# Kernel tuning notes

Hardware: AMD Instinct MI355X
Metric: run time of the kernel (lower is better)

Reference implementation:

```python
import jax, jax.numpy as jnp
import numpy as np

DIM = 128
HOP = 2
NEIGH = [12, 2]  # neighbor_num per hop
ALPHA = 0.2      # leaky-relu slope
NUM_NODE = 50000
B, S = 128, 50
STDV = 1.0 / np.sqrt(DIM)


def _leaky(x):
    return jnp.where(x >= 0, x, ALPHA * x)


def _local_agg(h, adj, a_local):
    # h: [B,S,D], adj: [B,S,S] ints in 0..4, a_local: [4,D]
    a_in = h[:, :, None, :] * h[:, None, :, :]            # [B,S,S,D]
    e = _leaky(jnp.einsum('bijd,kd->kbij', a_in, a_local))  # [4,B,S,S]
    att = jnp.full(adj.shape, -9e15, dtype=h.dtype)
    for k in range(4):
        att = jnp.where(adj == k + 1, e[k], att)
    att = jax.nn.softmax(att, axis=-1)
    return jnp.einsum('bij,bjd->bid', att, h)


def _global_agg(self_v, neigh_v, extra_v, w1, w2, w3, bias):
    # self_v: [B,N,D], neigh_v: [B,N,K,D], extra_v: [B,N,D]
    a = _leaky(jnp.einsum('bnkd,de->bnke', extra_v[:, :, None, :] * neigh_v, w1))
    a = jnp.einsum('bnke,e->bnk', a, w2)
    a = jax.nn.softmax(a, axis=-1)
    agg = jnp.einsum('bnk,bnkd->bnd', a, neigh_v)
    out = jnp.concatenate([self_v, agg], axis=-1) @ w3 + bias
    return jax.nn.relu(out)


def setup_inputs() -> dict:
    key = jax.random.key(0)
    ks = jax.random.split(key, 12)
    u = lambda k, shp: jax.random.uniform(k, shp, jnp.float32, -STDV, STDV)
    return {
        'inputs': jax.random.randint(ks[0], (B, S), 0, NUM_NODE),
        'adj': jax.random.randint(ks[1], (B, S, S), 0, 5),
        'mask_item': jnp.ones((B, S), dtype=jnp.int32),
        'item': jax.random.randint(ks[2], (B, S), 0, NUM_NODE),
        'first_adj': jax.random.randint(ks[3], (B, S * NEIGH[0]), 0, NUM_NODE),
        'adj_all': jax.random.randint(ks[4], (NUM_NODE, 2), 0, NUM_NODE),
        'embedding': u(ks[5], (NUM_NODE, DIM)),
        'a_local': u(ks[6], (4, DIM)),
        'gw1': u(ks[7], (HOP, DIM, DIM)),
        'gw2': u(ks[8], (HOP, DIM)),
        'gw3': u(ks[9], (HOP, 2 * DIM, DIM)),
        'gbias': u(ks[10], (HOP, DIM)),
    }


def reference(inputs, adj, mask_item, item, first_adj, adj_all,
              embedding, a_local, gw1, gw2, gw3, gbias):
    b, s = inputs.shape
    h = embedding[inputs]                                  # [B,S,D]
    h_local = _local_agg(h, adj, a_local)

    m = mask_item.astype(embedding.dtype)[..., None]       # [B,S,1]
    item_emb = embedding[item] * m
    sum_item = jnp.sum(item_emb, 1) / jnp.sum(m, 1)        # [B,D]
    sess = sum_item[:, None, :]                            # [B,1,D]

    # multi-hop neighbor sampling
    neigh1 = first_adj.reshape(b, s * NEIGH[0])            # [B, 600]
    neigh2 = adj_all[neigh1.reshape(-1)].reshape(b, s * NEIGH[0] * NEIGH[1])  # [B,1200]
    ev = [embedding[inputs], embedding[neigh1], embedding[neigh2]]

    for n_hop in range(HOP):
        nxt = []
        for hop in range(HOP - n_hop):
            neigh_v = ev[hop + 1].reshape(b, -1, NEIGH[hop], DIM)
            extra_v = jnp.broadcast_to(sess, (b, ev[hop].shape[1], DIM))
            nxt.append(_global_agg(ev[hop], neigh_v, extra_v,
                                   gw1[n_hop], gw2[n_hop], gw3[n_hop], gbias[n_hop]))
        ev = nxt
    h_global = ev[0].reshape(b, s, DIM)

    # dropout is identity at eval
    return h_local + h_global
```

## Files before the change

### kernel.cpp

```cpp
#include <hip/hip_runtime.h>
#include <stdint.h>

typedef unsigned short ushort_t;
typedef __attribute__((ext_vector_type(8))) short bf16x8;
typedef __attribute__((ext_vector_type(4))) float f32x4;

#define B_   128
#define S_   50
#define D_   128
#define ALPHA_ 0.2f

__device__ __forceinline__ float bf2f(ushort_t u){
  return __uint_as_float(((uint32_t)u) << 16);
}
__device__ __forceinline__ ushort_t f2bf(float f){
  uint32_t x = __float_as_uint(f);
  x = (x + 0x7fffu + ((x >> 16) & 1u)) >> 16;
  return (ushort_t)x;
}
__device__ __forceinline__ float leaky(float x){ return x >= 0.f ? x : ALPHA_*x; }

__device__ __forceinline__ int detect_flag_block(const uint32_t* __restrict__ emb_raw){
  __shared__ int flg;
  if (threadIdx.x == 0){
    int ok = 1;
    for (int i = 0; i < 64; i++){
      uint32_t lo = emb_raw[i] & 0xffffu;
      uint32_t ex = (lo >> 7) & 0xFFu;
      if (!(lo == 0u || (ex >= 64u && ex <= 126u))) ok = 0;
    }
    flg = ok;
  }
  __syncthreads();
  return flg;
}

__global__ void cvt_all(const void* __restrict__ p0, const void* __restrict__ p1,
                        const void* __restrict__ p2, const void* __restrict__ p3,
                        const void* __restrict__ p4, const void* __restrict__ p5,
                        ushort_t* __restrict__ dst){
  int flag = detect_flag_block((const uint32_t*)p0);
  const int seg_end[6] = {6400000, 6400512, 6433280, 6433536, 6499072, 6499328};
  int base = (blockIdx.x*256 + threadIdx.x) * 4;
  if (base >= 6499328) return;
  int s = 0;
  while (base >= seg_end[s]) s++;
  int segbase = (s == 0) ? 0 : seg_end[s-1];
  const void* src = (s==0)?p0:(s==1)?p1:(s==2)?p2:(s==3)?p3:(s==4)?p4:p5;
  int off = base - segbase;
  union { ushort_t u[4]; uint2 d2; } o;
  if (flag){
    o.d2 = *(const uint2*)((const ushort_t*)src + off);
  } else {
    float4 v = *(const float4*)((const float*)src + off);
    o.u[0] = f2bf(v.x); o.u[1] = f2bf(v.y); o.u[2] = f2bf(v.z); o.u[3] = f2bf(v.w);
  }
  *(uint2*)(dst + base) = o.d2;
}

__global__ void prep_frags(const void* __restrict__ emb_raw,
                           const void* __restrict__ w1r, const void* __restrict__ w3r,
                           uint4* __restrict__ w1f, uint4* __restrict__ w3f){
  int flag = detect_flag_block((const uint32_t*)emb_raw);
  int id = blockIdx.x*256 + threadIdx.x;
  if (id >= 12288) return;
  if (id < 4096){
    int h = id >> 11, i = id & 2047;
    int kt = i >> 9, rem = i & 511, t = rem >> 6, ln = rem & 63;
    int q = ln >> 4, c = ln & 15;
    union { ushort_t u[8]; uint4 q4; } e;
    #pragma unroll
    for (int j = 0; j < 8; j++){
      int idx = h*16384 + (32*kt + q*8 + j)*128 + 16*t + c;
      e.u[j] = flag ? ((const ushort_t*)w1r)[idx] : f2bf(((const float*)w1r)[idx]);
    }
    w1f[h*2048 + i] = e.q4;
  } else {
    int id2 = id - 4096;
    int h = id2 >> 12, i = id2 & 4095;
    int kt = i >> 9, rem = i & 511, t = rem >> 6, ln = rem & 63;
    int q = ln >> 4, c = ln & 15;
    union { ushort_t u[8]; uint4 q4; } e;
    #pragma unroll
    for (int j = 0; j < 8; j++){
      int idx = h*32768 + (32*kt + q*8 + j)*128 + 16*t + c;
      e.u[j] = flag ? ((const ushort_t*)w3r)[idx] : f2bf(((const float*)w3r)[idx]);
    }
    w3f[h*4096 + i] = e.q4;
  }
}

__global__ __launch_bounds__(256) void sess_local(
    const int* __restrict__ inputs, const int* __restrict__ adj,
    const int* __restrict__ item, const int* __restrict__ mask,
    const ushort_t* __restrict__ emb, const ushort_t* __restrict__ alocb,
    ushort_t* __restrict__ sessb, ushort_t* __restrict__ hlb){
  int blk = blockIdx.x;
  int tid = threadIdx.x;
  if (blk >= 512){
    int b = (blk - 512)*2 + (tid >> 7);
    int d = tid & 127;
    float acc = 0.f, den = 0.f;
    for (int s = 0; s < S_; s++){
      float fm = (float)mask[b*S_ + s];
      int id = item[b*S_ + s];
      acc += fm * bf2f(emb[(size_t)id*D_ + d]);
      den += fm;
    }
    sessb[b*D_ + d] = f2bf(acc / den);
    return;
  }
  __shared__ ushort_t hS[64][136];
  __shared__ float    attS[16][68];
  __shared__ int      sids[64];
  int b  = blk >> 2;
  int mi = blk & 3;
  if (tid < 64) sids[tid] = (tid < S_) ? inputs[b*S_ + tid] : 0;
  __syncthreads();
  for (int idx = tid; idx < 64*16; idx += 256){
    int j = idx >> 4, ch = idx & 15;
    uint4 v = {0u, 0u, 0u, 0u};
    if (j < S_) v = *(const uint4*)(emb + (size_t)sids[j]*D_ + ch*8);
    *(uint4*)(&hS[j][ch*8]) = v;
  }
  for (int idx = tid; idx < 16*64; idx += 256)
    attS[idx >> 6][idx & 63] = -9.0e15f;
  __syncthreads();

  int lane = tid & 63, wv = tid >> 6;
  int q = lane >> 4, c = lane & 15;

  f32x4 Eacc[4];
  #pragma unroll
  for (int ni = 0; ni < 4; ni++) Eacc[ni] = (f32x4){0.f,0.f,0.f,0.f};
  #pragma unroll
  for (int kt = 0; kt < 4; kt++){
    uint4 av = *(const uint4*)(alocb + wv*D_ + kt*32 + q*8);
    const uint32_t* ap = (const uint32_t*)&av;
    uint4 hv = *(const uint4*)(&hS[mi*16 + c][kt*32 + q*8]);
    const uint32_t* hp = (const uint32_t*)&hv;
    union { ushort_t u[8]; bf16x8 v; } afr;
    #pragma unroll
    for (int p = 0; p < 4; p++){
      float x0 = __uint_as_float(hp[p] << 16)         * __uint_as_float(ap[p] << 16);
      float x1 = __uint_as_float(hp[p] & 0xffff0000u) * __uint_as_float(ap[p] & 0xffff0000u);
      afr.u[2*p]   = f2bf(x0);
      afr.u[2*p+1] = f2bf(x1);
    }
    #pragma unroll
    for (int ni = 0; ni < 4; ni++){
      union { uint4 q4; bf16x8 v; } bfr;
      bfr.q4 = *(const uint4*)(&hS[ni*16 + c][kt*32 + q*8]);
      Eacc[ni] = __builtin_amdgcn_mfma_f32_16x16x32_bf16(afr.v, bfr.v, Eacc[ni], 0,0,0);
    }
  }
  const int* adjb = adj + (size_t)b*S_*S_;
  #pragma unroll
  for (int ni = 0; ni < 4; ni++){
    int j = ni*16 + c;
    #pragma unroll
    for (int r = 0; r < 4; r++){
      int i = mi*16 + q*4 + r;
      if (i < S_ && j < S_){
        int kk = adjb[i*S_ + j];
        if (kk == wv + 1) attS[q*4 + r][j] = leaky(Eacc[ni][r]);
      }
    }
  }
  __syncthreads();
  if (tid < 16){
    int i = mi*16 + tid;
    if (i < S_){
      float mx = -__builtin_inff();
      for (int j = 0; j < S_; j++) mx = fmaxf(mx, attS[tid][j]);
      float s = 0.f;
      for (int j = 0; j < S_; j++){ float e = __expf(attS[tid][j] - mx); attS[tid][j] = e; s += e; }
      float inv = 1.f / s;
      for (int j = 0; j < S_; j++) attS[tid][j] *= inv;
      for (int j = S_; j < 64; j++) attS[tid][j] = 0.f;
    } else {
      for (int j = 0; j < 64; j++) attS[tid][j] = 0.f;
    }
  }
  __syncthreads();
  f32x4 Pacc[2];
  Pacc[0] = (f32x4){0.f,0.f,0.f,0.f};
  Pacc[1] = (f32x4){0.f,0.f,0.f,0.f};
  #pragma unroll
  for (int kt = 0; kt < 2; kt++){
    union { ushort_t u[8]; bf16x8 v; } afr;
    const float* arow = &attS[c][kt*32 + q*8];
    #pragma unroll
    for (int j = 0; j < 8; j++) afr.u[j] = f2bf(arow[j]);
    #pragma unroll
    for (int nn = 0; nn < 2; nn++){
      int ni = 2*wv + nn;
      union { ushort_t u[8]; bf16x8 v; } bfr;
      #pragma unroll
      for (int jj = 0; jj < 8; jj++)
        bfr.u[jj] = hS[kt*32 + q*8 + jj][ni*16 + c];
      Pacc[nn] = __builtin_amdgcn_mfma_f32_16x16x32_bf16(afr.v, bfr.v, Pacc[nn], 0,0,0);
    }
  }
  #pragma unroll
  for (int nn = 0; nn < 2; nn++){
    int d = (2*wv + nn)*16 + c;
    #pragma unroll
    for (int r = 0; r < 4; r++){
      int i = mi*16 + q*4 + r;
      if (i < S_) hlb[((size_t)b*S_ + i)*D_ + d] = f2bf(Pacc[nn][r]);
    }
  }
}

__global__ __launch_bounds__(256) void score_mfma_ab(
    const ushort_t* __restrict__ sessb, const ushort_t* __restrict__ emb,
    const int* __restrict__ neigh1, const int* __restrict__ adj_all,
    const uint4* __restrict__ w1f, const ushort_t* __restrict__ w2,
    float* __restrict__ score, int nA){
  __shared__ uint4 bfrag[2048];
  int tid = threadIdx.x;
  for (int i = tid; i < 2048; i += 256) bfrag[i] = w1f[i];
  __syncthreads();
  int lane = tid & 63, wave = tid >> 6;
  int m = lane & 15, q = lane >> 4;
  float w2v[8];
  #pragma unroll
  for (int t = 0; t < 8; t++) w2v[t] = bf2f(w2[16*t + m]);

  for (int it = 0; it < 2; it++){
    int row_base = blockIdx.x*128 + it*64 + wave*16;
    int row = row_base + m;
    const ushort_t* nrow; int b;
    if (row < nA){
      nrow = emb + (size_t)neigh1[row]*D_;
      b = row / 600;
    } else {
      int r2 = row - nA;
      nrow = emb + (size_t)adj_all[(size_t)neigh1[r2>>1]*2 + (r2&1)]*D_;
      b = r2 / 1200;
    }
    const ushort_t* srow = sessb + (size_t)b*D_;

    f32x4 acc[8];
    #pragma unroll
    for (int t = 0; t < 8; t++) acc[t] = (f32x4){0.f,0.f,0.f,0.f};
    #pragma unroll
    for (int kt = 0; kt < 4; kt++){
      uint4 nv = *(const uint4*)(nrow + kt*32 + q*8);
      uint4 sv = *(const uint4*)(srow + kt*32 + q*8);
      const uint32_t* np = (const uint32_t*)&nv;
      const uint32_t* sp = (const uint32_t*)&sv;
      union { ushort_t u[8]; bf16x8 v; } afr;
      #pragma unroll
      for (int p = 0; p < 4; p++){
        uint32_t n2 = np[p], s2 = sp[p];
        float a0 = __uint_as_float(n2 << 16)          * __uint_as_float(s2 << 16);
        float a1 = __uint_as_float(n2 & 0xffff0000u)  * __uint_as_float(s2 & 0xffff0000u);
        afr.u[2*p]   = f2bf(a0);
        afr.u[2*p+1] = f2bf(a1);
      }
      #pragma unroll
      for (int t = 0; t < 8; t++){
        union { uint4 q4; bf16x8 v; } bfr;
        bfr.q4 = bfrag[(kt*8 + t)*64 + lane];
        acc[t] = __builtin_amdgcn_mfma_f32_16x16x32_bf16(afr.v, bfr.v, acc[t], 0, 0, 0);
      }
    }
    #pragma unroll
    for (int r = 0; r < 4; r++){
      float s = 0.f;
      #pragma unroll
      for (int t = 0; t < 8; t++) s += leaky(acc[t][r]) * w2v[t];
      s += __shfl_xor(s, 1, 64);
      s += __shfl_xor(s, 2, 64);
      s += __shfl_xor(s, 4, 64);
      s += __shfl_xor(s, 8, 64);
      if (m == 0) score[row_base + q*4 + r] = s;
    }
  }
}

__global__ __launch_bounds__(256) void score_mfma_c(
    const ushort_t* __restrict__ sessb, const ushort_t* __restrict__ out1,
    const uint4* __restrict__ w1f, const ushort_t* __restrict__ w2,
    float* __restrict__ score){
  __shared__ uint4 bfrag[2048];
  int tid = threadIdx.x;
  for (int i = tid; i < 2048; i += 256) bfrag[i] = w1f[i];
  __syncthreads();
  int lane = tid & 63, wave = tid >> 6;
  int m = lane & 15, q = lane >> 4;
  float w2v[8];
  #pragma unroll
  for (int t = 0; t < 8; t++) w2v[t] = bf2f(w2[16*t + m]);
  for (int it = 0; it < 2; it++){
    int row_base = blockIdx.x*128 + it*64 + wave*16;
    int row = row_base + m;
    const ushort_t* nrow = out1 + (size_t)row*D_;
    int b = row / 600;
    const ushort_t* srow = sessb + (size_t)b*D_;
    f32x4 acc[8];
    #pragma unroll
    for (int t = 0; t < 8; t++) acc[t] = (f32x4){0.f,0.f,0.f,0.f};
    #pragma unroll
    for (int kt = 0; kt < 4; kt++){
      uint4 nv = *(const uint4*)(nrow + kt*32 + q*8);
      uint4 sv = *(const uint4*)(srow + kt*32 + q*8);
      const uint32_t* np = (const uint32_t*)&nv;
      const uint32_t* sp = (const uint32_t*)&sv;
      union { ushort_t u[8]; bf16x8 v; } afr;
      #pragma unroll
      for (int p = 0; p < 4; p++){
        uint32_t n2 = np[p], s2 = sp[p];
        float a0 = __uint_as_float(n2 << 16)          * __uint_as_float(s2 << 16);
        float a1 = __uint_as_float(n2 & 0xffff0000u)  * __uint_as_float(s2 & 0xffff0000u);
        afr.u[2*p]   = f2bf(a0);
        afr.u[2*p+1] = f2bf(a1);
      }
      #pragma unroll
      for (int t = 0; t < 8; t++){
        union { uint4 q4; bf16x8 v; } bfr;
        bfr.q4 = bfrag[(kt*8 + t)*64 + lane];
        acc[t] = __builtin_amdgcn_mfma_f32_16x16x32_bf16(afr.v, bfr.v, acc[t], 0, 0, 0);
      }
    }
    #pragma unroll
    for (int r = 0; r < 4; r++){
      float s = 0.f;
      #pragma unroll
      for (int t = 0; t < 8; t++) s += leaky(acc[t][r]) * w2v[t];
      s += __shfl_xor(s, 1, 64);
      s += __shfl_xor(s, 2, 64);
      s += __shfl_xor(s, 4, 64);
      s += __shfl_xor(s, 8, 64);
      if (m == 0) score[row_base + q*4 + r] = s;
    }
  }
}

template<int K>
__device__ __forceinline__ void softmaxK(const float* __restrict__ sc, float att[K]){
  float mx = -__builtin_inff();
  #pragma unroll
  for (int k = 0; k < K; k++){ att[k] = sc[k]; mx = fmaxf(mx, att[k]); }
  float s = 0.f;
  #pragma unroll
  for (int k = 0; k < K; k++){ att[k] = __expf(att[k] - mx); s += att[k]; }
  float inv = 1.f / s;
  #pragma unroll
  for (int k = 0; k < K; k++) att[k] *= inv;
}

template<int K>
__device__ __forceinline__ void out_tile(
    int lane, const uint4* __restrict__ afrag,
    const ushort_t* __restrict__ sptr, const ushort_t* const nptr[K],
    const float att[K], f32x4 acc[8]){
  int q = lane >> 4;
  #pragma unroll
  for (int kt = 0; kt < 8; kt++){
    union { ushort_t u[8]; uint4 q4; bf16x8 v; } bfr;
    if (kt < 4){
      bfr.q4 = *(const uint4*)(sptr + kt*32 + q*8);
    } else {
      float g[8] = {0,0,0,0,0,0,0,0};
      #pragma unroll
      for (int k = 0; k < K; k++){
        uint4 nv = *(const uint4*)(nptr[k] + (kt-4)*32 + q*8);
        const uint32_t* np = (const uint32_t*)&nv;
        #pragma unroll
        for (int p = 0; p < 4; p++){
          g[2*p]   = fmaf(att[k], __uint_as_float(np[p] << 16),         g[2*p]);
          g[2*p+1] = fmaf(att[k], __uint_as_float(np[p] & 0xffff0000u), g[2*p+1]);
        }
      }
      #pragma unroll
      for (int j = 0; j < 8; j++) bfr.u[j] = f2bf(g[j]);
    }
    #pragma unroll
    for (int t = 0; t < 8; t++){
      union { uint4 q4; bf16x8 v; } af;
      af.q4 = afrag[(kt*8 + t)*64 + lane];
      acc[t] = __builtin_amdgcn_mfma_f32_16x16x32_bf16(af.v, bfr.v, acc[t], 0, 0, 0);
    }
  }
}

__global__ __launch_bounds__(512) void out_mfma_ab(
    const float* __restrict__ score, const int* __restrict__ idx,
    const int* __restrict__ nbr, const int* __restrict__ adj_all,
    const ushort_t* __restrict__ emb, const uint4* __restrict__ w3f,
    const ushort_t* __restrict__ bias,
    ushort_t* __restrict__ o0c, ushort_t* __restrict__ out1c,
    int nA, int nTot, int scoreBbase){
  __shared__ uint4 afrag[4096];
  int tid = threadIdx.x;
  for (int i = tid; i < 4096; i += 512) afrag[i] = w3f[i];
  __syncthreads();
  int lane = tid & 63, wave = tid >> 6;
  int mrow = lane & 15, q = lane >> 4;
  float bv[8][4];
  #pragma unroll
  for (int t = 0; t < 8; t++){
    const ushort_t* bp = bias + 16*t + q*4;
    #pragma unroll
    for (int r = 0; r < 4; r++) bv[t][r] = bf2f(bp[r]);
  }
  int row_base = blockIdx.x*128 + wave*16;
  int row = row_base + mrow;
  bool active = row < nTot;
  int rowc = active ? row : (nTot - 1);
  bool isA = rowc < nA;
  f32x4 acc[8];
  #pragma unroll
  for (int t = 0; t < 8; t++) acc[t] = (f32x4){0.f,0.f,0.f,0.f};
  if (isA){
    const ushort_t* sptr = emb + (size_t)idx[rowc]*D_;
    const ushort_t* nptr[12];
    #pragma unroll
    for (int k = 0; k < 12; k++) nptr[k] = emb + (size_t)nbr[rowc*12 + k]*D_;
    float att[12];
    softmaxK<12>(score + (size_t)rowc*12, att);
    out_tile<12>(lane, afrag, sptr, nptr, att, acc);
  } else {
    int rB = rowc - nA;
    const ushort_t* sptr = emb + (size_t)nbr[rB]*D_;
    const ushort_t* nptr[2];
    #pragma unroll
    for (int k = 0; k < 2; k++) nptr[k] = emb + (size_t)adj_all[(size_t)nbr[rB]*2 + k]*D_;
    float att[2];
    softmaxK<2>(score + scoreBbase + (size_t)rB*2, att);
    out_tile<2>(lane, afrag, sptr, nptr, att, acc);
  }
  if (active){
    ushort_t* dst = isA ? (o0c + (size_t)row*D_) : (out1c + (size_t)(row - nA)*D_);
    #pragma unroll
    for (int t = 0; t < 8; t++){
      int col0 = 16*t + q*4;
      union { ushort_t u[4]; uint2 d2; } pk;
      #pragma unroll
      for (int r = 0; r < 4; r++) pk.u[r] = f2bf(fmaxf(acc[t][r] + bv[t][r], 0.f));
      *(uint2*)(dst + col0) = pk.d2;
    }
  }
}

__global__ __launch_bounds__(512) void out_mfma_c(
    const float* __restrict__ score, const ushort_t* __restrict__ out1,
    const ushort_t* __restrict__ selfsrc, const uint4* __restrict__ w3f,
    const ushort_t* __restrict__ bias,
    const ushort_t* __restrict__ addsrc, float* __restrict__ outf, int nrows){
  __shared__ uint4 afrag[4096];
  int tid = threadIdx.x;
  for (int i = tid; i < 4096; i += 512) afrag[i] = w3f[i];
  __syncthreads();
  int lane = tid & 63, wave = tid >> 6;
  int mrow = lane & 15, q = lane >> 4;
  float bv[8][4];
  #pragma unroll
  for (int t = 0; t < 8; t++){
    const ushort_t* bp = bias + 16*t + q*4;
    #pragma unroll
    for (int r = 0; r < 4; r++) bv[t][r] = bf2f(bp[r]);
  }
  int row_base = blockIdx.x*128 + wave*16;
  int row = row_base + mrow;
  bool active = row < nrows;
  int rowc = active ? row : (nrows - 1);
  const ushort_t* sptr = selfsrc + (size_t)rowc*D_;
  const ushort_t* nptr[12];
  #pragma unroll
  for (int k = 0; k < 12; k++) nptr[k] = out1 + (size_t)(rowc*12 + k)*D_;
  float att[12];
  softmaxK<12>(score + (size_t)rowc*12, att);
  f32x4 acc[8];
  #pragma unroll
  for (int t = 0; t < 8; t++) acc[t] = (f32x4){0.f,0.f,0.f,0.f};
  out_tile<12>(lane, afrag, sptr, nptr, att, acc);
  if (active){
    #pragma unroll
    for (int t = 0; t < 8; t++){
      int col0 = 16*t + q*4;
      float v[4];
      const ushort_t* ap = addsrc + (size_t)row*D_ + col0;
      #pragma unroll
      for (int r = 0; r < 4; r++)
        v[r] = fmaxf(acc[t][r] + bv[t][r], 0.f) + bf2f(ap[r]);
      *(f32x4*)(outf + (size_t)row*D_ + col0) = (f32x4){v[0], v[1], v[2], v[3]};
    }
  }
}

extern "C" void kernel_launch(void* const* d_in, const int* in_sizes, int n_in,
                              void* d_out, int out_size, void* d_ws, size_t ws_size,
                              hipStream_t stream) {
  const int* inputs    = (const int*)d_in[0];
  const int* adj       = (const int*)d_in[1];
  const int* mask_item = (const int*)d_in[2];
  const int* item      = (const int*)d_in[3];
  const int* first_adj = (const int*)d_in[4];
  const int* adj_all   = (const int*)d_in[5];

  char* ws = (char*)d_ws;
  size_t o = 0;
  ushort_t* emb_b  = (ushort_t*)(ws + o); o += 12800000;
  ushort_t* alocb  = (ushort_t*)(ws + o); o += 1024;
  ushort_t* gw1b   = (ushort_t*)(ws + o); o += 65536;
  ushort_t* gw2b   = (ushort_t*)(ws + o); o += 512;
  ushort_t* gw3b   = (ushort_t*)(ws + o); o += 131072;
  ushort_t* gbb    = (ushort_t*)(ws + o); o += 512;
  ushort_t* sessb  = (ushort_t*)(ws + o); o += 32768;
  ushort_t* hlb    = (ushort_t*)(ws + o); o += 1638400;
  uint4*    w1f    = (uint4*)(ws + o);    o += 65536;
  uint4*    w3f    = (uint4*)(ws + o);    o += 131072;
  size_t fixed = o;
  (void)gw1b; (void)gw3b;
  int CHB = 16;
  if      (ws_size >= fixed + (size_t)128*173600) CHB = 128;
  else if (ws_size >= fixed + (size_t)64 *173600) CHB = 64;
  else if (ws_size >= fixed + (size_t)32 *173600) CHB = 32;
  ushort_t* out1c = (ushort_t*)(ws + o);  o += (size_t)CHB*153600;
  ushort_t* o0c   = (ushort_t*)(ws + o);  o += (size_t)CHB*12800;
  float*    score = (float*)(ws + o);

  float* outp = (float*)d_out;

  cvt_all<<<(6499328/4 + 255)/256, 256, 0, stream>>>(d_in[6], d_in[7], d_in[8], d_in[9],
                                                     d_in[10], d_in[11], emb_b);
  prep_frags<<<48, 256, 0, stream>>>(d_in[6], d_in[8], d_in[10], w1f, w3f);

  sess_local<<<576, 256, 0, stream>>>(inputs, adj, item, mask_item,
                                      emb_b, alocb, sessb, hlb);

  int nchunk = B_ / CHB;
  for (int c = 0; c < nchunk; c++){
    int b0 = c * CHB;
    const int* fadj  = first_adj + (size_t)b0 * 600;
    const ushort_t* sbc = sessb + (size_t)b0 * D_;
    ushort_t*  hlc   = hlb  + (size_t)b0 * 50 * D_;
    float*     outc  = outp + (size_t)b0 * 50 * D_;
    int nA600 = CHB*600, nA50 = CHB*50, nTot = CHB*650;

    score_mfma_ab<<<(3*nA600)/128, 256, 0, stream>>>(sbc, emb_b, fadj, adj_all,
                                                     w1f, gw2b, score, nA600);
    out_mfma_ab<<<(nTot + 127)/128, 512, 0, stream>>>(score, inputs + b0*50, fadj, adj_all,
                                                      emb_b, w3f, gbb, o0c, out1c,
                                                      nA50, nTot, nA600);
    score_mfma_c<<<nA600/128, 256, 0, stream>>>(sbc, out1c, w1f + 2048, gw2b + 128, score);
    out_mfma_c<<<(nA50 + 127)/128, 512, 0, stream>>>(score, out1c, o0c,
                                                     w3f + 4096, gbb + 128,
                                                     hlc, outc, nA50);
  }
}
```

Baseline: 199.4 us.

## Precompute per-node W3 projections and fuse setup kernels into one launch

Merges the conversion, fragment-prep, session-mean and local-attention kernels into a single launch. The local and session blocks now read the raw embedding directly instead of waiting for the converted copy. It also adds a path that projects every embedding row through both halves of W3 up front (Tt, Tb), so hop-0 output becomes a softmax-weighted gather of projected rows instead of a per-row MFMA. That path projects all 50k nodes rather than only the gathered ones, and needs extra workspace; when workspace is short it falls back to the old chunked path.

```diff
diff --git a/kernel.cpp b/kernel.cpp
--- a/kernel.cpp
+++ b/kernel.cpp
@@ -35,180 +35,259 @@
   return flg;
 }
 
-__global__ void cvt_all(const void* __restrict__ p0, const void* __restrict__ p1,
-                        const void* __restrict__ p2, const void* __restrict__ p3,
-                        const void* __restrict__ p4, const void* __restrict__ p5,
-                        ushort_t* __restrict__ dst){
-  int flag = detect_flag_block((const uint32_t*)p0);
-  const int seg_end[6] = {6400000, 6400512, 6433280, 6433536, 6499072, 6499328};
-  int base = (blockIdx.x*256 + threadIdx.x) * 4;
-  if (base >= 6499328) return;
-  int s = 0;
-  while (base >= seg_end[s]) s++;
-  int segbase = (s == 0) ? 0 : seg_end[s-1];
-  const void* src = (s==0)?p0:(s==1)?p1:(s==2)?p2:(s==3)?p3:(s==4)?p4:p5;
-  int off = base - segbase;
-  union { ushort_t u[4]; uint2 d2; } o;
-  if (flag){
-    o.d2 = *(const uint2*)((const ushort_t*)src + off);
-  } else {
-    float4 v = *(const float4*)((const float*)src + off);
-    o.u[0] = f2bf(v.x); o.u[1] = f2bf(v.y); o.u[2] = f2bf(v.z); o.u[3] = f2bf(v.w);
-  }
-  *(uint2*)(dst + base) = o.d2;
-}
-
-__global__ void prep_frags(const void* __restrict__ emb_raw,
-                           const void* __restrict__ w1r, const void* __restrict__ w3r,
-                           uint4* __restrict__ w1f, uint4* __restrict__ w3f){
-  int flag = detect_flag_block((const uint32_t*)emb_raw);
-  int id = blockIdx.x*256 + threadIdx.x;
-  if (id >= 12288) return;
-  if (id < 4096){
-    int h = id >> 11, i = id & 2047;
-    int kt = i >> 9, rem = i & 511, t = rem >> 6, ln = rem & 63;
-    int q = ln >> 4, c = ln & 15;
-    union { ushort_t u[8]; uint4 q4; } e;
-    #pragma unroll
-    for (int j = 0; j < 8; j++){
-      int idx = h*16384 + (32*kt + q*8 + j)*128 + 16*t + c;
-      e.u[j] = flag ? ((const ushort_t*)w1r)[idx] : f2bf(((const float*)w1r)[idx]);
-    }
-    w1f[h*2048 + i] = e.q4;
-  } else {
-    int id2 = id - 4096;
-    int h = id2 >> 12, i = id2 & 4095;
-    int kt = i >> 9, rem = i & 511, t = rem >> 6, ln = rem & 63;
-    int q = ln >> 4, c = ln & 15;
-    union { ushort_t u[8]; uint4 q4; } e;
-    #pragma unroll
-    for (int j = 0; j < 8; j++){
-      int idx = h*32768 + (32*kt + q*8 + j)*128 + 16*t + c;
-      e.u[j] = flag ? ((const ushort_t*)w3r)[idx] : f2bf(((const float*)w3r)[idx]);
-    }
-    w3f[h*4096 + i] = e.q4;
-  }
-}
-
-__global__ __launch_bounds__(256) void sess_local(
+#define NLOCAL_ 512
+#define NSESS_  64
+#define NCVT_   6347
+#define NPREP_  48
+
+__global__ __launch_bounds__(256) void k1(
     const int* __restrict__ inputs, const int* __restrict__ adj,
     const int* __restrict__ item, const int* __restrict__ mask,
-    const ushort_t* __restrict__ emb, const ushort_t* __restrict__ alocb,
-    ushort_t* __restrict__ sessb, ushort_t* __restrict__ hlb){
-  int blk = blockIdx.x;
-  int tid = threadIdx.x;
-  if (blk >= 512){
-    int b = (blk - 512)*2 + (tid >> 7);
+    const void* __restrict__ p0, const void* __restrict__ p1,
+    const void* __restrict__ p2, const void* __restrict__ p3,
+    const void* __restrict__ p4, const void* __restrict__ p5,
+    ushort_t* __restrict__ emb_b, uint4* __restrict__ w1f, uint4* __restrict__ w3f,
+    ushort_t* __restrict__ sessb, ushort_t* __restrict__ hlb)
+{
+  int blk = blockIdx.x, tid = threadIdx.x;
+  int flag = detect_flag_block((const uint32_t*)p0);
+
+  if (blk < NLOCAL_){
+    __shared__ ushort_t hS[64][136];
+    __shared__ float    attS[16][68];
+    __shared__ int      sids[64];
+    __shared__ ushort_t alS[512];
+    int b  = blk >> 2;
+    int mi = blk & 3;
+    if (tid < 64) sids[tid] = (tid < S_) ? inputs[b*S_ + tid] : 0;
+    for (int i = tid; i < 512; i += 256)
+      alS[i] = flag ? ((const ushort_t*)p1)[i] : f2bf(((const float*)p1)[i]);
+    __syncthreads();
+    if (flag){
+      const ushort_t* e16 = (const ushort_t*)p0;
+      for (int idx = tid; idx < 64*16; idx += 256){
+        int j = idx >> 4, ch = idx & 15;
+        uint4 v = {0u, 0u, 0u, 0u};
+        if (j < S_) v = *(const uint4*)(e16 + (size_t)sids[j]*D_ + ch*8);
+        *(uint4*)(&hS[j][ch*8]) = v;
+      }
+    } else {
+      const float* ef = (const float*)p0;
+      for (int idx = tid; idx < 64*32; idx += 256){
+        int j = idx >> 5, ch = idx & 31;
+        union { ushort_t u[4]; uint2 d2; } o;
+        o.d2 = make_uint2(0u, 0u);
+        if (j < S_){
+          float4 v = *(const float4*)(ef + (size_t)sids[j]*D_ + ch*4);
+          o.u[0]=f2bf(v.x); o.u[1]=f2bf(v.y); o.u[2]=f2bf(v.z); o.u[3]=f2bf(v.w);
+        }
+        *(uint2*)(&hS[j][ch*4]) = o.d2;
+      }
+    }
+    for (int idx = tid; idx < 16*64; idx += 256)
+      attS[idx >> 6][idx & 63] = -9.0e15f;
+    __syncthreads();
+
+    int lane = tid & 63, wv = tid >> 6;
+    int q = lane >> 4, c = lane & 15;
+
+    f32x4 Eacc[4];
+    #pragma unroll
+    for (int ni = 0; ni < 4; ni++) Eacc[ni] = (f32x4){0.f,0.f,0.f,0.f};
+    #pragma unroll
+    for (int kt = 0; kt < 4; kt++){
+      uint4 av = *(const uint4*)(alS + wv*D_ + kt*32 + q*8);
+      const uint32_t* ap = (const uint32_t*)&av;
+      uint4 hv = *(const uint4*)(&hS[mi*16 + c][kt*32 + q*8]);
+      const uint32_t* hp = (const uint32_t*)&hv;
+      union { ushort_t u[8]; bf16x8 v; } afr;
+      #pragma unroll
+      for (int p = 0; p < 4; p++){
+        float x0 = __uint_as_float(hp[p] << 16)         * __uint_as_float(ap[p] << 16);
+        float x1 = __uint_as_float(hp[p] & 0xffff0000u) * __uint_as_float(ap[p] & 0xffff0000u);
+        afr.u[2*p]   = f2bf(x0);
+        afr.u[2*p+1] = f2bf(x1);
+      }
+      #pragma unroll
+      for (int ni = 0; ni < 4; ni++){
+        union { uint4 q4; bf16x8 v; } bfr;
+        bfr.q4 = *(const uint4*)(&hS[ni*16 + c][kt*32 + q*8]);
+        Eacc[ni] = __builtin_amdgcn_mfma_f32_16x16x32_bf16(afr.v, bfr.v, Eacc[ni], 0,0,0);
+      }
+    }
+    const int* adjb = adj + (size_t)b*S_*S_;
+    #pragma unroll
+    for (int ni = 0; ni < 4; ni++){
+      int j = ni*16 + c;
+      #pragma unroll
+      for (int r = 0; r < 4; r++){
+        int i = mi*16 + q*4 + r;
+        if (i < S_ && j < S_){
+          int kk = adjb[i*S_ + j];
+          if (kk == wv + 1) attS[q*4 + r][j] = leaky(Eacc[ni][r]);
+        }
+      }
+    }
+    __syncthreads();
+    {
+      int r  = tid >> 4;
+      int cg = tid & 15;
+      int i  = mi*16 + r;
+      float v0 = attS[r][cg*4+0], v1 = attS[r][cg*4+1];
+      float v2 = attS[r][cg*4+2], v3 = attS[r][cg*4+3];
+      float mx = fmaxf(fmaxf(v0,v1), fmaxf(v2,v3));
+      #pragma unroll
+      for (int off = 1; off < 16; off <<= 1) mx = fmaxf(mx, __shfl_xor(mx, off, 16));
+      float e0 = (cg*4+0 < S_) ? __expf(v0 - mx) : 0.f;
+      float e1 = (cg*4+1 < S_) ? __expf(v1 - mx) : 0.f;
+      float e2 = (cg*4+2 < S_) ? __expf(v2 - mx) : 0.f;
+      float e3 = (cg*4+3 < S_) ? __expf(v3 - mx) : 0.f;
+      float s = e0 + e1 + e2 + e3;
+      #pragma unroll
+      for (int off = 1; off < 16; off <<= 1) s += __shfl_xor(s, off, 16);
+      float inv = (i < S_) ? 1.f / s : 0.f;
+      attS[r][cg*4+0] = e0*inv;
+      attS[r][cg*4+1] = e1*inv;
+      attS[r][cg*4+2] = e2*inv;
+      attS[r][cg*4+3] = e3*inv;
+    }
+    __syncthreads();
+    f32x4 Pacc[2];
+    Pacc[0] = (f32x4){0.f,0.f,0.f,0.f};
+    Pacc[1] = (f32x4){0.f,0.f,0.f,0.f};
+    #pragma unroll
+    for (int kt = 0; kt < 2; kt++){
+      union { ushort_t u[8]; bf16x8 v; } afr;
+      const float* arow = &attS[c][kt*32 + q*8];
+      #pragma unroll
+      for (int j = 0; j < 8; j++) afr.u[j] = f2bf(arow[j]);
+      #pragma unroll
+      for (int nn = 0; nn < 2; nn++){
+        int ni = 2*wv + nn;
+        union { ushort_t u[8]; bf16x8 v; } bfr;
+        #pragma unroll
+        for (int jj = 0; jj < 8; jj++)
+          bfr.u[jj] = hS[kt*32 + q*8 + jj][ni*16 + c];
+        Pacc[nn] = __builtin_amdgcn_mfma_f32_16x16x32_bf16(afr.v, bfr.v, Pacc[nn], 0,0,0);
+      }
+    }
+    #pragma unroll
+    for (int nn = 0; nn < 2; nn++){
+      int d = (2*wv + nn)*16 + c;
+      #pragma unroll
+      for (int r = 0; r < 4; r++){
+        int i = mi*16 + q*4 + r;
+        if (i < S_) hlb[((size_t)b*S_ + i)*D_ + d] = f2bf(Pacc[nn][r]);
+      }
+    }
+  } else if (blk < NLOCAL_ + NSESS_){
+    int b = (blk - NLOCAL_)*2 + (tid >> 7);
     int d = tid & 127;
     float acc = 0.f, den = 0.f;
-    for (int s = 0; s < S_; s++){
-      float fm = (float)mask[b*S_ + s];
-      int id = item[b*S_ + s];
-      acc += fm * bf2f(emb[(size_t)id*D_ + d]);
-      den += fm;
+    if (flag){
+      const ushort_t* e16 = (const ushort_t*)p0;
+      for (int s = 0; s < S_; s++){
+        float fm = (float)mask[b*S_ + s];
+        int id = item[b*S_ + s];
+        acc += fm * bf2f(e16[(size_t)id*D_ + d]);
+        den += fm;
+      }
+    } else {
+      const float* ef = (const float*)p0;
+      for (int s = 0; s < S_; s++){
+        float fm = (float)mask[b*S_ + s];
+        int id = item[b*S_ + s];
+        acc += fm * ef[(size_t)id*D_ + d];
+        den += fm;
+      }
     }
     sessb[b*D_ + d] = f2bf(acc / den);
-    return;
-  }
-  __shared__ ushort_t hS[64][136];
-  __shared__ float    attS[16][68];
-  __shared__ int      sids[64];
-  int b  = blk >> 2;
-  int mi = blk & 3;
-  if (tid < 64) sids[tid] = (tid < S_) ? inputs[b*S_ + tid] : 0;
+  } else if (blk < NLOCAL_ + NSESS_ + NCVT_){
+    const int seg_end[6] = {6400000, 6400512, 6433280, 6433536, 6499072, 6499328};
+    int base = ((blk - NLOCAL_ - NSESS_)*256 + tid) * 4;
+    if (base >= 6499328) return;
+    int s = 0;
+    while (base >= seg_end[s]) s++;
+    int segbase = (s == 0) ? 0 : seg_end[s-1];
+    const void* src = (s==0)?p0:(s==1)?p1:(s==2)?p2:(s==3)?p3:(s==4)?p4:p5;
+    int off = base - segbase;
+    union { ushort_t u[4]; uint2 d2; } o;
+    if (flag){
+      o.d2 = *(const uint2*)((const ushort_t*)src + off);
+    } else {
+      float4 v = *(const float4*)((const float*)src + off);
+      o.u[0] = f2bf(v.x); o.u[1] = f2bf(v.y); o.u[2] = f2bf(v.z); o.u[3] = f2bf(v.w);
+    }
+    *(uint2*)(emb_b + base) = o.d2;
+  } else {
+    int id = (blk - NLOCAL_ - NSESS_ - NCVT_)*256 + tid;
+    if (id >= 12288) return;
+    if (id < 4096){
+      int h = id >> 11, i = id & 2047;
+      int kt = i >> 9, rem = i & 511, t = rem >> 6, ln = rem & 63;
+      int q = ln >> 4, c = ln & 15;
+      union { ushort_t u[8]; uint4 q4; } e;
+      #pragma unroll
+      for (int j = 0; j < 8; j++){
+        int idx = h*16384 + (32*kt + q*8 + j)*128 + 16*t + c;
+        e.u[j] = flag ? ((const ushort_t*)p2)[idx] : f2bf(((const float*)p2)[idx]);
+      }
+      w1f[h*2048 + i] = e.q4;
+    } else {
+      int id2 = id - 4096;
+      int h = id2 >> 12, i = id2 & 4095;
+      int kt = i >> 9, rem = i & 511, t = rem >> 6, ln = rem & 63;
+      int q = ln >> 4, c = ln & 15;
+      union { ushort_t u[8]; uint4 q4; } e;
+      #pragma unroll
+      for (int j = 0; j < 8; j++){
+        int idx = h*32768 + (32*kt + q*8 + j)*128 + 16*t + c;
+        e.u[j] = flag ? ((const ushort_t*)p4)[idx] : f2bf(((const float*)p4)[idx]);
+      }
+      w3f[h*4096 + i] = e.q4;
+    }
+  }
+}
+
+__global__ __launch_bounds__(512) void tprep(
+    const ushort_t* __restrict__ emb, const uint4* __restrict__ w3f,
+    ushort_t* __restrict__ Tt, ushort_t* __restrict__ Tb)
+{
+  __shared__ uint4 frag[4096];
+  int tid = threadIdx.x;
+  for (int i = tid; i < 4096; i += 512) frag[i] = w3f[i];
   __syncthreads();
-  for (int idx = tid; idx < 64*16; idx += 256){
-    int j = idx >> 4, ch = idx & 15;
-    uint4 v = {0u, 0u, 0u, 0u};
-    if (j < S_) v = *(const uint4*)(emb + (size_t)sids[j]*D_ + ch*8);
-    *(uint4*)(&hS[j][ch*8]) = v;
-  }
-  for (int idx = tid; idx < 16*64; idx += 256)
-    attS[idx >> 6][idx & 63] = -9.0e15f;
-  __syncthreads();
-
-  int lane = tid & 63, wv = tid >> 6;
-  int q = lane >> 4, c = lane & 15;
-
-  f32x4 Eacc[4];
-  #pragma unroll
-  for (int ni = 0; ni < 4; ni++) Eacc[ni] = (f32x4){0.f,0.f,0.f,0.f};
+  int lane = tid & 63, wave = tid >> 6;
+  int m = lane & 15, q = lane >> 4;
+  int row = blockIdx.x*128 + wave*16 + m;
+  int rowc = row < 50000 ? row : 49999;
+  f32x4 acct[8], accb[8];
+  #pragma unroll
+  for (int t = 0; t < 8; t++){ acct[t] = (f32x4){0.f,0.f,0.f,0.f}; accb[t] = (f32x4){0.f,0.f,0.f,0.f}; }
   #pragma unroll
   for (int kt = 0; kt < 4; kt++){
-    uint4 av = *(const uint4*)(alocb + wv*D_ + kt*32 + q*8);
-    const uint32_t* ap = (const uint32_t*)&av;
-    uint4 hv = *(const uint4*)(&hS[mi*16 + c][kt*32 + q*8]);
-    const uint32_t* hp = (const uint32_t*)&hv;
-    union { ushort_t u[8]; bf16x8 v; } afr;
-    #pragma unroll
-    for (int p = 0; p < 4; p++){
-      float x0 = __uint_as_float(hp[p] << 16)         * __uint_as_float(ap[p] << 16);
-      float x1 = __uint_as_float(hp[p] & 0xffff0000u) * __uint_as_float(ap[p] & 0xffff0000u);
-      afr.u[2*p]   = f2bf(x0);
-      afr.u[2*p+1] = f2bf(x1);
-    }
-    #pragma unroll
-    for (int ni = 0; ni < 4; ni++){
-      union { uint4 q4; bf16x8 v; } bfr;
-      bfr.q4 = *(const uint4*)(&hS[ni*16 + c][kt*32 + q*8]);
-      Eacc[ni] = __builtin_amdgcn_mfma_f32_16x16x32_bf16(afr.v, bfr.v, Eacc[ni], 0,0,0);
-    }
-  }
-  const int* adjb = adj + (size_t)b*S_*S_;
-  #pragma unroll
-  for (int ni = 0; ni < 4; ni++){
-    int j = ni*16 + c;
-    #pragma unroll
-    for (int r = 0; r < 4; r++){
-      int i = mi*16 + q*4 + r;
-      if (i < S_ && j < S_){
-        int kk = adjb[i*S_ + j];
-        if (kk == wv + 1) attS[q*4 + r][j] = leaky(Eacc[ni][r]);
-      }
-    }
-  }
-  __syncthreads();
-  if (tid < 16){
-    int i = mi*16 + tid;
-    if (i < S_){
-      float mx = -__builtin_inff();
-      for (int j = 0; j < S_; j++) mx = fmaxf(mx, attS[tid][j]);
-      float s = 0.f;
-      for (int j = 0; j < S_; j++){ float e = __expf(attS[tid][j] - mx); attS[tid][j] = e; s += e; }
-      float inv = 1.f / s;
-      for (int j = 0; j < S_; j++) attS[tid][j] *= inv;
-      for (int j = S_; j < 64; j++) attS[tid][j] = 0.f;
-    } else {
-      for (int j = 0; j < 64; j++) attS[tid][j] = 0.f;
-    }
-  }
-  __syncthreads();
-  f32x4 Pacc[2];
-  Pacc[0] = (f32x4){0.f,0.f,0.f,0.f};
-  Pacc[1] = (f32x4){0.f,0.f,0.f,0.f};
-  #pragma unroll
-  for (int kt = 0; kt < 2; kt++){
-    union { ushort_t u[8]; bf16x8 v; } afr;
-    const float* arow = &attS[c][kt*32 + q*8];
-    #pragma unroll
-    for (int j = 0; j < 8; j++) afr.u[j] = f2bf(arow[j]);
-    #pragma unroll
-    for (int nn = 0; nn < 2; nn++){
-      int ni = 2*wv + nn;
-      union { ushort_t u[8]; bf16x8 v; } bfr;
-      #pragma unroll
-      for (int jj = 0; jj < 8; jj++)
-        bfr.u[jj] = hS[kt*32 + q*8 + jj][ni*16 + c];
-      Pacc[nn] = __builtin_amdgcn_mfma_f32_16x16x32_bf16(afr.v, bfr.v, Pacc[nn], 0,0,0);
-    }
-  }
-  #pragma unroll
-  for (int nn = 0; nn < 2; nn++){
-    int d = (2*wv + nn)*16 + c;
-    #pragma unroll
-    for (int r = 0; r < 4; r++){
-      int i = mi*16 + q*4 + r;
-      if (i < S_) hlb[((size_t)b*S_ + i)*D_ + d] = f2bf(Pacc[nn][r]);
+    union { uint4 q4; bf16x8 v; } bfr;
+    bfr.q4 = *(const uint4*)(emb + (size_t)rowc*D_ + kt*32 + q*8);
+    #pragma unroll
+    for (int t = 0; t < 8; t++){
+      union { uint4 q4; bf16x8 v; } af, af2;
+      af.q4  = frag[(kt*8 + t)*64 + lane];
+      af2.q4 = frag[((kt+4)*8 + t)*64 + lane];
+      acct[t] = __builtin_amdgcn_mfma_f32_16x16x32_bf16(af.v,  bfr.v, acct[t], 0, 0, 0);
+      accb[t] = __builtin_amdgcn_mfma_f32_16x16x32_bf16(af2.v, bfr.v, accb[t], 0, 0, 0);
+    }
+  }
+  if (row < 50000){
+    #pragma unroll
+    for (int t = 0; t < 8; t++){
+      int col0 = 16*t + q*4;
+      union { ushort_t u[4]; uint2 d2; } pk;
+      #pragma unroll
+      for (int r = 0; r < 4; r++) pk.u[r] = f2bf(acct[t][r]);
+      *(uint2*)(Tt + (size_t)row*D_ + col0) = pk.d2;
+      #pragma unroll
+      for (int r = 0; r < 4; r++) pk.u[r] = f2bf(accb[t][r]);
+      *(uint2*)(Tb + (size_t)row*D_ + col0) = pk.d2;
     }
   }
 }
@@ -385,6 +464,56 @@
       acc[t] = __builtin_amdgcn_mfma_f32_16x16x32_bf16(af.v, bfr.v, acc[t], 0, 0, 0);
     }
   }
+}
+
+__global__ __launch_bounds__(256) void gather_out(
+    const int* __restrict__ idx, const int* __restrict__ nbr,
+    const int* __restrict__ adj_all, const float* __restrict__ score,
+    const ushort_t* __restrict__ Tt, const ushort_t* __restrict__ Tb,
+    const ushort_t* __restrict__ bias,
+    ushort_t* __restrict__ o0c, ushort_t* __restrict__ out1c,
+    int nA50, int nTot, int scoreBbase)
+{
+  int row  = (blockIdx.x*256 + threadIdx.x) >> 6;
+  int lane = threadIdx.x & 63;
+  if (row >= nTot) return;
+  row = __builtin_amdgcn_readfirstlane(row);
+  float b0 = bf2f(bias[lane*2]), b1 = bf2f(bias[lane*2 + 1]);
+  float acc0, acc1;
+  ushort_t* dst;
+  if (row < nA50){
+    float att[12];
+    softmaxK<12>(score + (size_t)row*12, att);
+    uint32_t sv = *(const uint32_t*)(Tt + (size_t)idx[row]*D_ + lane*2);
+    acc0 = __uint_as_float(sv << 16);
+    acc1 = __uint_as_float(sv & 0xffff0000u);
+    #pragma unroll
+    for (int k = 0; k < 12; k++){
+      uint32_t nv = *(const uint32_t*)(Tb + (size_t)nbr[row*12 + k]*D_ + lane*2);
+      acc0 = fmaf(att[k], __uint_as_float(nv << 16),          acc0);
+      acc1 = fmaf(att[k], __uint_as_float(nv & 0xffff0000u),  acc1);
+    }
+    dst = o0c + (size_t)row*D_;
+  } else {
+    int rB = row - nA50;
+    float att[2];
+    softmaxK<2>(score + scoreBbase + (size_t)rB*2, att);
+    int self = nbr[rB];
+    uint32_t sv = *(const uint32_t*)(Tt + (size_t)self*D_ + lane*2);
+    acc0 = __uint_as_float(sv << 16);
+    acc1 = __uint_as_float(sv & 0xffff0000u);
+    #pragma unroll
+    for (int k = 0; k < 2; k++){
+      uint32_t nv = *(const uint32_t*)(Tb + (size_t)adj_all[(size_t)self*2 + k]*D_ + lane*2);
+      acc0 = fmaf(att[k], __uint_as_float(nv << 16),          acc0);
+      acc1 = fmaf(att[k], __uint_as_float(nv & 0xffff0000u),  acc1);
+    }
+    dst = out1c + (size_t)rB*D_;
+  }
+  union { ushort_t u[2]; uint32_t d; } pk;
+  pk.u[0] = f2bf(fmaxf(acc0 + b0, 0.f));
+  pk.u[1] = f2bf(fmaxf(acc1 + b1, 0.f));
+  *(uint32_t*)(dst + lane*2) = pk.d;
 }
 
 __global__ __launch_bounds__(512) void out_mfma_ab(
@@ -515,41 +644,64 @@
   uint4*    w1f    = (uint4*)(ws + o);    o += 65536;
   uint4*    w3f    = (uint4*)(ws + o);    o += 131072;
   size_t fixed = o;
-  (void)gw1b; (void)gw3b;
-  int CHB = 16;
-  if      (ws_size >= fixed + (size_t)128*173600) CHB = 128;
-  else if (ws_size >= fixed + (size_t)64 *173600) CHB = 64;
-  else if (ws_size >= fixed + (size_t)32 *173600) CHB = 32;
-  ushort_t* out1c = (ushort_t*)(ws + o);  o += (size_t)CHB*153600;
-  ushort_t* o0c   = (ushort_t*)(ws + o);  o += (size_t)CHB*12800;
-  float*    score = (float*)(ws + o);
+  (void)alocb; (void)gw1b; (void)gw3b;
 
   float* outp = (float*)d_out;
 
-  cvt_all<<<(6499328/4 + 255)/256, 256, 0, stream>>>(d_in[6], d_in[7], d_in[8], d_in[9],
-                                                     d_in[10], d_in[11], emb_b);
-  prep_frags<<<48, 256, 0, stream>>>(d_in[6], d_in[8], d_in[10], w1f, w3f);
-
-  sess_local<<<576, 256, 0, stream>>>(inputs, adj, item, mask_item,
-                                      emb_b, alocb, sessb, hlb);
-
-  int nchunk = B_ / CHB;
-  for (int c = 0; c < nchunk; c++){
-    int b0 = c * CHB;
-    const int* fadj  = first_adj + (size_t)b0 * 600;
-    const ushort_t* sbc = sessb + (size_t)b0 * D_;
-    ushort_t*  hlc   = hlb  + (size_t)b0 * 50 * D_;
-    float*     outc  = outp + (size_t)b0 * 50 * D_;
-    int nA600 = CHB*600, nA50 = CHB*50, nTot = CHB*650;
-
-    score_mfma_ab<<<(3*nA600)/128, 256, 0, stream>>>(sbc, emb_b, fadj, adj_all,
+  k1<<<NLOCAL_ + NSESS_ + NCVT_ + NPREP_, 256, 0, stream>>>(
+      inputs, adj, item, mask_item,
+      d_in[6], d_in[7], d_in[8], d_in[9], d_in[10], d_in[11],
+      emb_b, w1f, w3f, sessb, hlb);
+
+  const size_t TPATH_NEED = fixed + 2*(size_t)12800000
+                          + (size_t)128*153600
+                          + (size_t)128*12800
+                          + (size_t)3*128*600*4;
+  if (ws_size >= TPATH_NEED){
+    ushort_t* Tt    = (ushort_t*)(ws + o);  o += 12800000;
+    ushort_t* Tb    = (ushort_t*)(ws + o);  o += 12800000;
+    ushort_t* out1c = (ushort_t*)(ws + o);  o += (size_t)128*153600;
+    ushort_t* o0c   = (ushort_t*)(ws + o);  o += (size_t)128*12800;
+    float*    score = (float*)(ws + o);
+    int nA600 = 128*600, nA50 = 128*50, nTot = 128*650;
+
+    tprep<<<391, 512, 0, stream>>>(emb_b, w3f, Tt, Tb);
+    score_mfma_ab<<<(3*nA600)/128, 256, 0, stream>>>(sessb, emb_b, first_adj, adj_all,
                                                      w1f, gw2b, score, nA600);
-    out_mfma_ab<<<(nTot + 127)/128, 512, 0, stream>>>(score, inputs + b0*50, fadj, adj_all,
-                                                      emb_b, w3f, gbb, o0c, out1c,
-                                                      nA50, nTot, nA600);
-    score_mfma_c<<<nA600/128, 256, 0, stream>>>(sbc, out1c, w1f + 2048, gw2b + 128, score);
+    gather_out<<<(nTot*64 + 255)/256, 256, 0, stream>>>(inputs, first_adj, adj_all, score,
+                                                        Tt, Tb, gbb, o0c, out1c,
+                                                        nA50, nTot, nA600);
+    score_mfma_c<<<nA600/128, 256, 0, stream>>>(sessb, out1c, w1f + 2048, gw2b + 128, score);
     out_mfma_c<<<(nA50 + 127)/128, 512, 0, stream>>>(score, out1c, o0c,
                                                      w3f + 4096, gbb + 128,
-                                                     hlc, outc, nA50);
-  }
-}
+                                                     hlb, outp, nA50);
+  } else {
+    int CHB = 16;
+    if      (ws_size >= fixed + (size_t)128*173600) CHB = 128;
+    else if (ws_size >= fixed + (size_t)64 *173600) CHB = 64;
+    else if (ws_size >= fixed + (size_t)32 *173600) CHB = 32;
+    ushort_t* out1c = (ushort_t*)(ws + o);  o += (size_t)CHB*153600;
+    ushort_t* o0c   = (ushort_t*)(ws + o);  o += (size_t)CHB*12800;
+    float*    score = (float*)(ws + o);
+
+    int nchunk = B_ / CHB;
+    for (int c = 0; c < nchunk; c++){
+      int b0 = c * CHB;
+      const int* fadj  = first_adj + (size_t)b0 * 600;
+      const ushort_t* sbc = sessb + (size_t)b0 * D_;
+      ushort_t*  hlc   = hlb  + (size_t)b0 * 50 * D_;
+      float*     outc  = outp + (size_t)b0 * 50 * D_;
+      int nA600 = CHB*600, nA50 = CHB*50, nTot = CHB*650;
+
+      score_mfma_ab<<<(3*nA600)/128, 256, 0, stream>>>(sbc, emb_b, fadj, adj_all,
+                                                       w1f, gw2b, score, nA600);
+      out_mfma_ab<<<(nTot + 127)/128, 512, 0, stream>>>(score, inputs + b0*50, fadj, adj_all,
+                                                        emb_b, w3f, gbb, o0c, out1c,
+                                                        nA50, nTot, nA600);
+      score_mfma_c<<<nA600/128, 256, 0, stream>>>(sbc, out1c, w1f + 2048, gw2b + 128, score);
+      out_mfma_c<<<(nA50 + 127)/128, 512, 0, stream>>>(score, out1c, o0c,
+                                                       w3f + 4096, gbb + 128,
+                                                       hlc, outc, nA50);
+    }
+  }
+}
```

After: 194.0 us. 2.7% less time.
